# Kernel optimization log

Measured on AMD Instinct MI355X. Metric: run time of the kernel, lower is better.

Reference implementation:

```python
import jax, jax.numpy as jnp
import numpy as np

N, E, G = 20000, 160000, 32          # nodes, edges, graphs in batch
F_IN, H, P, C = 67, 2048, 1024, 18   # in_feat, hidden_feat, fc2 width, n_classifier
EPS = 1e-5
SLOPE = 0.01  # leaky_relu default negative slope


def setup_inputs() -> dict:
    key = jax.random.key(0)
    ks = jax.random.split(key, 24)
    w = lambda k, shape: (jax.random.normal(k, shape, jnp.float32) * 0.02)
    return {
        "h": jax.random.normal(ks[0], (N, F_IN), jnp.float32),
        "src": jax.random.randint(ks[1], (E,), 0, N),
        "dst": jax.random.randint(ks[2], (E,), 0, N),
        "gids": jnp.sort(jax.random.randint(ks[3], (N,), 0, G)),
        # SAGEConv layers: fc_self, fc_neigh (no per-fc bias), shared bias
        "ws1": w(ks[4], (F_IN, H)), "wn1": w(ks[5], (F_IN, H)), "b1": jnp.zeros((H,), jnp.float32),
        "ws2": w(ks[6], (H, H)),    "wn2": w(ks[7], (H, H)),    "b2": jnp.zeros((H,), jnp.float32),
        "ws3": w(ks[8], (H, H)),    "wn3": w(ks[9], (H, H)),    "b3": jnp.zeros((H,), jnp.float32),
        # batch norms (gamma, beta)
        "g1": jnp.ones((H,), jnp.float32), "be1": jnp.zeros((H,), jnp.float32),
        "g2": jnp.ones((H,), jnp.float32), "be2": jnp.zeros((H,), jnp.float32),
        "g3": jnp.ones((H,), jnp.float32), "be3": jnp.zeros((H,), jnp.float32),
        # MLP head
        "fw1": w(ks[10], (H, H)), "fb1": jnp.zeros((H,), jnp.float32),
        "fw2": w(ks[11], (H, P)), "fb2": jnp.zeros((P,), jnp.float32),
        "fw3": w(ks[12], (P, C)), "fb3": jnp.zeros((C,), jnp.float32),
    }


def _leaky(x):
    return jnp.where(x >= 0, x, SLOPE * x)


def _sage(x, src, dst, w_self, w_neigh, b):
    # DGL SAGEConv 'mean': mean of neighbor (src) features into dst, then linears.
    nsum = jax.ops.segment_sum(x[src], dst, num_segments=N)            # [N, F]
    deg = jax.ops.segment_sum(jnp.ones((E,), x.dtype), dst, num_segments=N)
    neigh = nsum / jnp.maximum(deg, 1.0)[:, None]                      # 0 for isolated
    return x @ w_self + neigh @ w_neigh + b


def _bn(x, gamma, beta):
    m = x.mean(0)
    v = x.var(0)
    return (x - m) * jax.lax.rsqrt(v + EPS) * gamma + beta


def reference(h, src, dst, gids,
              ws1, wn1, b1, g1, be1,
              ws2, wn2, b2, g2, be2,
              ws3, wn3, b3, g3, be3,
              fw1, fb1, fw2, fb2, fw3, fb3):
    x = _leaky(_bn(_sage(h, src, dst, ws1, wn1, b1), g1, be1))
    x = _leaky(_bn(_sage(x, src, dst, ws2, wn2, b2), g2, be2))
    x = _leaky(_bn(_sage(x, src, dst, ws3, wn3, b3), g3, be3))
    # mean pooling per graph
    gsum = jax.ops.segment_sum(x, gids, num_segments=G)                # [G, H]
    cnt = jax.ops.segment_sum(jnp.ones((N,), x.dtype), gids, num_segments=G)
    hg = gsum / jnp.maximum(cnt, 1.0)[:, None]
    # dropouts are identity in eval
    y = _leaky(hg @ fw1 + fb1)
    y = _leaky(y @ fw2 + fb2)
    return y @ fw3 + fb3
```

## Files before the change

### kernel.cpp

```cpp
#include <hip/hip_runtime.h>

typedef unsigned short u16;
typedef __attribute__((ext_vector_type(4))) float f32x4;
typedef __attribute__((ext_vector_type(8))) __bf16 bf16x8;
typedef __attribute__((ext_vector_type(8))) short s16x8;
typedef __attribute__((ext_vector_type(4))) u16 u16x4;

#define N_NODES 20000
#define N_EDGES 160000
#define N_GRAPH 32
#define F_IN 67
#define HID 2048
#define PW 1024
#define NCLS 18
#define MPAD 20096
#define MPAD2 20224
#define K1 192

__device__ __forceinline__ float bf2f(u16 u) {
    unsigned v = ((unsigned)u) << 16;
    float f; __builtin_memcpy(&f, &v, 4); return f;
}
__device__ __forceinline__ u16 f2bf(float f) {
    unsigned u; __builtin_memcpy(&u, &f, 4);
    u = (u + 0x7FFF + ((u >> 16) & 1)) >> 16;
    return (u16)u;
}
__device__ __forceinline__ int imax(int a, int b) { return a > b ? a : b; }

__device__ __forceinline__ void ld16(const u16* gptr, u16* lptr) {
    __builtin_amdgcn_global_load_lds(
        (const __attribute__((address_space(1))) unsigned int*)gptr,
        (__attribute__((address_space(3))) unsigned int*)lptr,
        16, 0, 0);
}

__global__ void k_hist(const int* __restrict__ dst, int* __restrict__ cnt) {
    int e = blockIdx.x * 256 + threadIdx.x;
    if (e < N_EDGES) atomicAdd(&cnt[dst[e]], 1);
}

__global__ void k_scan(const int* __restrict__ cnt, int* __restrict__ rowptr) {
    __shared__ int part[256];
    int t = threadIdx.x;
    const int per = (N_NODES + 255) / 256;
    int base = t * per;
    int s = 0;
    for (int i = 0; i < per; i++) { int idx = base + i; if (idx < N_NODES) s += cnt[idx]; }
    part[t] = s; __syncthreads();
    for (int off = 1; off < 256; off <<= 1) {
        int v = (t >= off) ? part[t - off] : 0;
        __syncthreads();
        part[t] += v;
        __syncthreads();
    }
    int running = (t == 0) ? 0 : part[t - 1];
    for (int i = 0; i < per; i++) {
        int idx = base + i;
        if (idx < N_NODES) { rowptr[idx] = running; running += cnt[idx]; }
    }
    if (t == 255) rowptr[N_NODES] = running;
}

__global__ void k_scatter(const int* __restrict__ src, const int* __restrict__ dst,
                          const int* __restrict__ rowptr, int* __restrict__ cursor,
                          int* __restrict__ csr) {
    int e = blockIdx.x * 256 + threadIdx.x;
    if (e < N_EDGES) {
        int d = dst[e];
        int p = atomicAdd(&cursor[d], 1);
        csr[rowptr[d] + p] = src[e];
    }
}

__global__ void k_w1t(const float* __restrict__ ws1, const float* __restrict__ wn1,
                      u16* __restrict__ w1t) {
    int n = blockIdx.x, t = threadIdx.x;
    float v = 0.f;
    if (t < F_IN) v = ws1[(size_t)t * HID + n];
    else if (t < 2 * F_IN) v = wn1[(size_t)(t - F_IN) * HID + n];
    w1t[(size_t)n * K1 + t] = f2bf(v);
}

__global__ void k_transpose2(const float* __restrict__ s0, const float* __restrict__ s1,
                             u16* __restrict__ dst) {
    __shared__ float tile[32][33];
    const float* src = blockIdx.z ? s1 : s0;
    int colofs = blockIdx.z ? HID : 0;
    int bx = blockIdx.x * 32, by = blockIdx.y * 32;
    int tx = threadIdx.x, ty = threadIdx.y;
#pragma unroll
    for (int i = 0; i < 32; i += 8)
        tile[ty + i][tx] = src[(size_t)(by + ty + i) * HID + bx + tx];
    __syncthreads();
#pragma unroll
    for (int i = 0; i < 32; i += 8)
        dst[(size_t)(bx + ty + i) * (2 * HID) + colofs + by + tx] = f2bf(tile[tx][ty + i]);
}

__global__ void k_agg1(const float* __restrict__ h, const int* __restrict__ rowptr,
                       const int* __restrict__ csr, u16* __restrict__ acat) {
    int n = blockIdx.x, t = threadIdx.x;
    if (t < F_IN) {
        acat[(size_t)n * K1 + t] = f2bf(h[(size_t)n * F_IN + t]);
    } else if (t < 2 * F_IN) {
        int c = t - F_IN;
        int e0 = rowptr[n], e1 = rowptr[n + 1];
        float a = 0.f;
        for (int e = e0; e < e1; e++) a += h[(size_t)csr[e] * F_IN + c];
        acat[(size_t)n * K1 + F_IN + c] = f2bf(a / (float)imax(e1 - e0, 1));
    }
}

__global__ __launch_bounds__(256)
void k_agg(const u16* __restrict__ x, const int* __restrict__ rowptr,
           const int* __restrict__ csr, u16* __restrict__ out) {
    int n = blockIdx.x, t = threadIdx.x;
    int e0 = rowptr[n], e1 = rowptr[n + 1];
    float acc[8] = {0, 0, 0, 0, 0, 0, 0, 0};
    for (int e = e0; e < e1; e++) {
        int s = csr[e];
        s16x8 v = *(const s16x8*)&x[(size_t)s * HID + t * 8];
#pragma unroll
        for (int j = 0; j < 8; j++) acc[j] += bf2f((u16)v[j]);
    }
    float inv = 1.0f / (float)imax(e1 - e0, 1);
    s16x8 o;
#pragma unroll
    for (int j = 0; j < 8; j++) o[j] = (short)f2bf(acc[j] * inv);
    *(s16x8*)&out[(size_t)n * HID + t * 8] = o;
}

__global__ __launch_bounds__(256)
void k_gemm(const u16* __restrict__ A0, const u16* __restrict__ A1, int ksplit,
            const u16* __restrict__ WT, u16* __restrict__ C,
            int ldA, int K, int ldC) {
    __shared__ u16 As[128 * 64];
    __shared__ u16 Bs[128 * 64];
    const int tid = threadIdx.x;
    const int lane = tid & 63;
    const int wave = tid >> 6;
    const int wr = (wave >> 1) * 64;
    const int wc = (wave & 1) * 64;
    const int lr = lane & 15;
    const int lk = (lane >> 4) * 8;
    const size_t row0 = (size_t)blockIdx.x * 128;
    const int col0 = blockIdx.y * 128;

    f32x4 acc[4][4];
#pragma unroll
    for (int i = 0; i < 4; i++)
#pragma unroll
        for (int j = 0; j < 4; j++) acc[i][j] = f32x4{0.f, 0.f, 0.f, 0.f};

    int rr[4], cc[4], lo[4];
#pragma unroll
    for (int i = 0; i < 4; i++) {
        int chunk = i * 256 + tid;
        rr[i] = chunk >> 3;
        cc[i] = (chunk & 7) * 8;
        lo[i] = (i * 256 + (wave << 6)) * 8;
    }
    size_t abase[4], bbase[4];
#pragma unroll
    for (int i = 0; i < 4; i++) {
        abase[i] = (row0 + rr[i]) * (size_t)ldA + cc[i];
        bbase[i] = ((size_t)col0 + rr[i]) * (size_t)K + cc[i];
    }

    for (int kt = 0; kt < K; kt += 64) {
        const u16* Asrc; int kc;
        if (kt < ksplit) { Asrc = A0; kc = kt; } else { Asrc = A1; kc = kt - ksplit; }
#pragma unroll
        for (int i = 0; i < 4; i++) {
            ld16(Asrc + abase[i] + kc, &As[lo[i]]);
            ld16(WT + bbase[i] + kt, &Bs[lo[i]]);
        }
        __syncthreads();
#pragma unroll
        for (int kk = 0; kk < 2; kk++) {
            bf16x8 af[4], bw[4];
#pragma unroll
            for (int i = 0; i < 4; i++)
                af[i] = *(const bf16x8*)&As[(wr + i * 16 + lr) * 64 + kk * 32 + lk];
#pragma unroll
            for (int j = 0; j < 4; j++)
                bw[j] = *(const bf16x8*)&Bs[(wc + j * 16 + lr) * 64 + kk * 32 + lk];
#pragma unroll
            for (int i = 0; i < 4; i++)
#pragma unroll
                for (int j = 0; j < 4; j++)
                    acc[i][j] = __builtin_amdgcn_mfma_f32_16x16x32_bf16(bw[j], af[i], acc[i][j], 0, 0, 0);
        }
        __syncthreads();
    }
#pragma unroll
    for (int i = 0; i < 4; i++) {
        size_t m = row0 + wr + i * 16 + lr;
#pragma unroll
        for (int j = 0; j < 4; j++) {
            int nb = col0 + wc + j * 16 + (lane >> 4) * 4;
            u16x4 o;
#pragma unroll
            for (int rg = 0; rg < 4; rg++) o[rg] = f2bf(acc[i][j][rg]);
            *(u16x4*)&C[m * (size_t)ldC + nb] = o;
        }
    }
}

#define VM4 asm volatile("s_waitcnt vmcnt(4)" ::: "memory")
#define VM2 asm volatile("s_waitcnt vmcnt(2)" ::: "memory")
#define VM0 asm volatile("s_waitcnt vmcnt(0)" ::: "memory")

#define STAGE_A(H) { const u16* as_ = (kt1 < 32 ? A0 : A1);                        \
    size_t ko_ = (size_t)(kt1 & 31) * 64 + swe;                                     \
    ld16(as_ + (row0 + 0 * 128 + (H) * 64 + r8) * 2048 + ko_,                       \
         LA + dbo + ((H) * 128 + 0 * 64 + r8) * 64 + ld8);                          \
    ld16(as_ + (row0 + 1 * 128 + (H) * 64 + r8) * 2048 + ko_,                       \
         LA + dbo + ((H) * 128 + 1 * 64 + r8) * 64 + ld8); }

#define STAGE_B(H) { size_t ko_ = (size_t)kt1 * 64 + swe;                           \
    ld16(WT + ((size_t)col0 + ((r8 >> 5)) * 64 + (H) * 32 + (r8 & 31)) * 4096 + ko_,\
         LB + dbo + ((H) * 128 + 0 * 64 + r8) * 64 + ld8);                          \
    ld16(WT + ((size_t)col0 + (2 + (r8 >> 5)) * 64 + (H) * 32 + (r8 & 31)) * 4096 + ko_,\
         LB + dbo + ((H) * 128 + 1 * 64 + r8) * 64 + ld8); }

#define RD_A(QM) {                                                                  \
    _Pragma("unroll") for (int f = 0; f < 4; ++f)                                   \
      _Pragma("unroll") for (int kk = 0; kk < 2; ++kk)                              \
        af[f][kk] = *(const bf16x8*)(bA + (QM) * 16384 + (wm * 64 + f * 16 + lr) * 128 \
                                     + ((kk * 64 + lg * 16) ^ rxor)); }

#define RD_B(DST, QN) {                                                             \
    _Pragma("unroll") for (int n = 0; n < 2; ++n)                                   \
      _Pragma("unroll") for (int kk = 0; kk < 2; ++kk)                              \
        DST[n][kk] = *(const bf16x8*)(bB + (QN) * 16384 + (wn * 32 + n * 16 + lr) * 128 \
                                     + ((kk * 64 + lg * 16) ^ rxor)); }

#define SYNC_MM(QM, QN, BW) {                                                       \
    __builtin_amdgcn_s_barrier();                                                   \
    __builtin_amdgcn_s_setprio(1);                                                  \
    _Pragma("unroll") for (int kk = 0; kk < 2; ++kk)                                \
      _Pragma("unroll") for (int f = 0; f < 4; ++f)                                 \
        _Pragma("unroll") for (int n = 0; n < 2; ++n)                               \
          acc[(QM) * 4 + f][(QN) * 2 + n] = __builtin_amdgcn_mfma_f32_16x16x32_bf16(\
              BW[n][kk], af[f][kk], acc[(QM) * 4 + f][(QN) * 2 + n], 0, 0, 0);      \
    __builtin_amdgcn_s_setprio(0); }

__global__ __launch_bounds__(512, 2)
void k_gemm256(const u16* __restrict__ A0, const u16* __restrict__ A1,
               const u16* __restrict__ WT, u16* __restrict__ C) {
    __shared__ u16 LA[2 * 256 * 64];
    __shared__ u16 LB[2 * 256 * 64];
    const int tid = threadIdx.x;
    const int lane = tid & 63;
    const int wave = tid >> 6;
    const int wm = wave >> 2, wn = wave & 3;
    const int lr = lane & 15, lg = lane >> 4;
    const int rxor = (lr & 7) << 4;

    const int g = (blockIdx.x & 7) * 79 + (blockIdx.x >> 3);
    const size_t row0 = (size_t)(g >> 3) * 256;
    const int col0 = (g & 7) * 256;

    const int r8 = tid >> 3;
    const int ld8 = (tid & 7) * 8;
    const int swe = ((ld8 * 2) ^ ((r8 & 7) << 4)) >> 1;

    f32x4 acc[8][4];
#pragma unroll
    for (int i = 0; i < 8; i++)
#pragma unroll
        for (int j = 0; j < 4; j++) acc[i][j] = f32x4{0.f, 0.f, 0.f, 0.f};

    {
        const int kt1 = 0; const int dbo = 0;
        STAGE_A(0) STAGE_B(0) STAGE_B(1) STAGE_A(1)
    }
    VM0;
    __builtin_amdgcn_s_barrier();

    bf16x8 af[4][2], bw[2][2], bw2[2][2];

    for (int t = 0; t < 63; ++t) {
        const char* bA = (const char*)LA + (t & 1) * 32768;
        const char* bB = (const char*)LB + (t & 1) * 32768;
        const int kt1 = t + 1;
        const int dbo = ((t + 1) & 1) * 16384;
        RD_A(0) RD_B(bw, 0) STAGE_A(0) VM4; SYNC_MM(0, 0, bw)
        RD_B(bw2, 1) STAGE_B(0) VM4; SYNC_MM(0, 1, bw2)
        RD_A(1) STAGE_B(1) SYNC_MM(1, 1, bw2)
        RD_B(bw, 0) STAGE_A(1) VM4; SYNC_MM(1, 0, bw)
    }
    {
        const char* bA = (const char*)LA + 32768;
        const char* bB = (const char*)LB + 32768;
        RD_A(0) RD_B(bw, 0) VM2; SYNC_MM(0, 0, bw)
        RD_B(bw2, 1) VM0; SYNC_MM(0, 1, bw2)
        RD_A(1) SYNC_MM(1, 1, bw2)
        RD_B(bw, 0) SYNC_MM(1, 0, bw)
    }

#pragma unroll
    for (int f = 0; f < 8; ++f) {
        size_t m = row0 + wm * 128 + f * 16 + lr;
#pragma unroll
        for (int n = 0; n < 4; ++n) {
            int cb = col0 + wn * 64 + n * 16 + lg * 4;
            u16x4 o;
#pragma unroll
            for (int rg = 0; rg < 4; ++rg) o[rg] = f2bf(acc[f][n][rg]);
            *(u16x4*)&C[m * HID + cb] = o;
        }
    }
}

__global__ __launch_bounds__(256)
void k_stats(const u16* __restrict__ x, float* __restrict__ ssum, float* __restrict__ ssq) {
    int t = threadIdx.x;
    int r0 = blockIdx.x * 100;
    float s[8] = {}, s2[8] = {};
    for (int i = 0; i < 100; ++i) {
        s16x8 v = *(const s16x8*)&x[(size_t)(r0 + i) * HID + t * 8];
#pragma unroll
        for (int j = 0; j < 8; ++j) { float f = bf2f((u16)v[j]); s[j] += f; s2[j] += f * f; }
    }
#pragma unroll
    for (int j = 0; j < 8; ++j) {
        atomicAdd(&ssum[t * 8 + j], s[j]);
        atomicAdd(&ssq[t * 8 + j], s2[j]);
    }
}

__global__ void k_bnleaky(const u16* __restrict__ xin,
                          const float* __restrict__ ssum, const float* __restrict__ ssq,
                          const float* __restrict__ gma, const float* __restrict__ bta,
                          u16* __restrict__ xout) {
    size_t eb = ((size_t)blockIdx.x * 256 + threadIdx.x) * 8;
    int col = (int)(eb & (HID - 1));
    s16x8 v = *(const s16x8*)&xin[eb];
    s16x8 o;
#pragma unroll
    for (int hq = 0; hq < 2; ++hq) {
        f32x4 su = *(const f32x4*)&ssum[col + hq * 4];
        f32x4 sq = *(const f32x4*)&ssq[col + hq * 4];
        f32x4 gm = *(const f32x4*)&gma[col + hq * 4];
        f32x4 bt = *(const f32x4*)&bta[col + hq * 4];
#pragma unroll
        for (int j = 0; j < 4; ++j) {
            float m = su[j] * (1.0f / N_NODES);
            float var = sq[j] * (1.0f / N_NODES) - m * m;
            float a = gm[j] * rsqrtf(var + 1e-5f);
            float d = bt[j] - m * a;
            float f = bf2f((u16)v[hq * 4 + j]) * a + d;
            f = f > 0.f ? f : 0.01f * f;
            o[hq * 4 + j] = (short)f2bf(f);
        }
    }
    *(s16x8*)&xout[eb] = o;
}

__global__ void k_bounds(const int* __restrict__ gids, int* __restrict__ gstart) {
    int t = threadIdx.x;
    if (t > N_GRAPH) return;
    int lo = 0, hi = N_NODES;
    while (lo < hi) { int mid = (lo + hi) >> 1; if (gids[mid] < t) lo = mid + 1; else hi = mid; }
    gstart[t] = lo;
}

__global__ void k_pool(const u16* __restrict__ x, const int* __restrict__ gstart,
                       float* __restrict__ hg) {
    int g = blockIdx.x;
    int col = blockIdx.y * 256 + threadIdx.x;
    int r0 = gstart[g], r1 = gstart[g + 1];
    float s = 0.f;
    for (int r = r0; r < r1; r++) s += bf2f(x[(size_t)r * HID + col]);
    hg[(size_t)g * HID + col] = s / (float)imax(r1 - r0, 1);
}

__global__ __launch_bounds__(256)
void k_mlp_part(const float* __restrict__ X, const float* __restrict__ W,
                float* __restrict__ Yp, int K, int Nc) {
    __shared__ float xs[32 * 256];
    int t = threadIdx.x;
    int kc = blockIdx.y;
    int n = blockIdx.x * 64 + (t & 63);
    int mg = t >> 6;
#pragma unroll
    for (int l = 0; l < 32; ++l) {
        int e = l * 256 + t;
        xs[e] = X[(size_t)(e >> 8) * K + kc * 256 + (e & 255)];
    }
    __syncthreads();
    float acc[8] = {};
    for (int k = 0; k < 256; ++k) {
        float wv = W[(size_t)(kc * 256 + k) * Nc + n];
#pragma unroll
        for (int i = 0; i < 8; ++i) acc[i] += xs[(mg * 8 + i) * 256 + k] * wv;
    }
#pragma unroll
    for (int i = 0; i < 8; ++i)
        Yp[(size_t)(kc * 32 + mg * 8 + i) * Nc + n] = acc[i];
}

__global__ void k_mlp_red(const float* __restrict__ Yp, const float* __restrict__ bias,
                          float* __restrict__ Y, int Nc, int leaky) {
    int idx = blockIdx.x * 256 + threadIdx.x;
    int n = idx % Nc;
    float s = 0.f;
#pragma unroll
    for (int kc = 0; kc < 8; ++kc) s += Yp[(size_t)kc * 32 * Nc + idx];
    float v = s + bias[n];
    if (leaky) v = v > 0.f ? v : 0.01f * v;
    Y[idx] = v;
}

__global__ void k_fc3(const float* __restrict__ y2, const float* __restrict__ fw3,
                      const float* __restrict__ fb3, float* __restrict__ out) {
    __shared__ float red[8][32];
    int m = blockIdx.x, t = threadIdx.x;
    int ch = t >> 5, c = t & 31;
    float s = 0.f;
    if (c < NCLS) {
        for (int j = 0; j < 128; ++j) {
            int k = ch * 128 + j;
            s += y2[(size_t)m * PW + k] * fw3[(size_t)k * NCLS + c];
        }
    }
    red[ch][c] = s;
    __syncthreads();
    if (t < NCLS) {
        float a = 0.f;
#pragma unroll
        for (int c2 = 0; c2 < 8; ++c2) a += red[c2][t];
        out[m * NCLS + t] = a + fb3[t];
    }
}

extern "C" void kernel_launch(void* const* d_in, const int* in_sizes, int n_in,
                              void* d_out, int out_size, void* d_ws, size_t ws_size,
                              hipStream_t stream) {
    const float* h   = (const float*)d_in[0];
    const int* src   = (const int*)d_in[1];
    const int* dst   = (const int*)d_in[2];
    const int* gids  = (const int*)d_in[3];
    const float* ws1 = (const float*)d_in[4];
    const float* wn1 = (const float*)d_in[5];
    const float* ws2 = (const float*)d_in[7];
    const float* wn2 = (const float*)d_in[8];
    const float* ws3 = (const float*)d_in[10];
    const float* wn3 = (const float*)d_in[11];
    const float* g1  = (const float*)d_in[13];
    const float* be1 = (const float*)d_in[14];
    const float* g2  = (const float*)d_in[15];
    const float* be2 = (const float*)d_in[16];
    const float* g3  = (const float*)d_in[17];
    const float* be3 = (const float*)d_in[18];
    const float* fw1 = (const float*)d_in[19];
    const float* fb1 = (const float*)d_in[20];
    const float* fw2 = (const float*)d_in[21];
    const float* fb2 = (const float*)d_in[22];
    const float* fw3 = (const float*)d_in[23];
    const float* fb3 = (const float*)d_in[24];
    float* out = (float*)d_out;
    (void)in_sizes; (void)n_in; (void)out_size;

    char* base = (char*)d_ws;
    size_t off = 0;
    auto alloc = [&](size_t b) -> char* {
        char* p = base + off;
        off += (b + 255) & ~(size_t)255;
        return p;
    };
    u16* BUF0 = (u16*)alloc((size_t)MPAD2 * HID * 2);
    u16* BUF1 = (u16*)alloc((size_t)MPAD2 * HID * 2);
    u16* BUF2 = (u16*)alloc((size_t)MPAD2 * HID * 2);
    u16* WT   = (u16*)alloc((size_t)HID * 2 * HID * 2);
    int* cnt    = (int*)alloc(N_NODES * 4);
    int* rowptr = (int*)alloc((N_NODES + 1) * 4);
    int* cursor = (int*)alloc(N_NODES * 4);
    int* csr    = (int*)alloc(N_EDGES * 4);
    float* ssum = (float*)alloc(HID * 4);
    float* ssq  = (float*)alloc(HID * 4);
    int* gstart = (int*)alloc(64 * 4);
    float* hg = (float*)alloc((size_t)N_GRAPH * HID * 4);
    float* y1 = (float*)alloc((size_t)N_GRAPH * HID * 4);
    float* y2 = (float*)alloc((size_t)N_GRAPH * PW * 4);
    u16* ACAT = (u16*)((char*)BUF2);
    u16* W1T  = (u16*)((char*)BUF2 + (size_t)MPAD * K1 * 2);
    float* Yp = (float*)((char*)BUF2);

    if (off > ws_size) return;

    hipMemsetAsync(cnt, 0, N_NODES * 4, stream);
    hipMemsetAsync(cursor, 0, N_NODES * 4, stream);
    hipMemsetAsync(ACAT, 0, (size_t)MPAD * K1 * 2, stream);

    k_hist<<<(N_EDGES + 255) / 256, 256, 0, stream>>>(dst, cnt);
    k_scan<<<1, 256, 0, stream>>>(cnt, rowptr);
    k_scatter<<<(N_EDGES + 255) / 256, 256, 0, stream>>>(src, dst, rowptr, cursor, csr);

    k_w1t<<<HID, K1, 0, stream>>>(ws1, wn1, W1T);
    k_agg1<<<N_NODES, 192, 0, stream>>>(h, rowptr, csr, ACAT);

    dim3 gg(MPAD / 128, HID / 128);
    dim3 tb(32, 8);
    k_gemm<<<gg, 256, 0, stream>>>(ACAT, ACAT, K1, W1T, BUF0, K1, K1, HID);
    hipMemsetAsync(ssum, 0, 2 * HID * 4, stream);
    k_stats<<<200, 256, 0, stream>>>(BUF0, ssum, ssq);
    k_bnleaky<<<20000, 256, 0, stream>>>(BUF0, ssum, ssq, g1, be1, BUF1);
    k_transpose2<<<dim3(64, 64, 2), tb, 0, stream>>>(ws2, wn2, WT);
    k_agg<<<N_NODES, 256, 0, stream>>>(BUF1, rowptr, csr, BUF2);
    k_gemm256<<<632, 512, 0, stream>>>(BUF1, BUF2, WT, BUF0);
    hipMemsetAsync(ssum, 0, 2 * HID * 4, stream);
    k_stats<<<200, 256, 0, stream>>>(BUF0, ssum, ssq);
    k_bnleaky<<<20000, 256, 0, stream>>>(BUF0, ssum, ssq, g2, be2, BUF1);
    k_transpose2<<<dim3(64, 64, 2), tb, 0, stream>>>(ws3, wn3, WT);
    k_agg<<<N_NODES, 256, 0, stream>>>(BUF1, rowptr, csr, BUF2);
    k_gemm256<<<632, 512, 0, stream>>>(BUF1, BUF2, WT, BUF0);
    hipMemsetAsync(ssum, 0, 2 * HID * 4, stream);
    k_stats<<<200, 256, 0, stream>>>(BUF0, ssum, ssq);
    k_bnleaky<<<20000, 256, 0, stream>>>(BUF0, ssum, ssq, g3, be3, BUF1);
    k_bounds<<<1, 64, 0, stream>>>(gids, gstart);
    k_pool<<<dim3(N_GRAPH, HID / 256), 256, 0, stream>>>(BUF1, gstart, hg);
    k_mlp_part<<<dim3(HID / 64, 8), 256, 0, stream>>>(hg, fw1, Yp, HID, HID);
    k_mlp_red<<<(N_GRAPH * HID) / 256, 256, 0, stream>>>(Yp, fb1, y1, HID, 1);
    k_mlp_part<<<dim3(PW / 64, 8), 256, 0, stream>>>(y1, fw2, Yp, HID, PW);
    k_mlp_red<<<(N_GRAPH * PW) / 256, 256, 0, stream>>>(Yp, fb2, y2, PW, 1);
    k_fc3<<<N_GRAPH, 256, 0, stream>>>(y2, fw3, fb3, out);
}
```

Measured before the change: 1.553 ms.

## Fuse batch-norm statistics into GEMM epilogue and reuse 256-tile GEMM for layer one

New measurement: 1.408 ms. 1.1x faster.

```diff
diff --git a/kernel.cpp b/kernel.cpp
--- a/kernel.cpp
+++ b/kernel.cpp
@@ -13,7 +13,6 @@
 #define HID 2048
 #define PW 1024
 #define NCLS 18
-#define MPAD 20096
 #define MPAD2 20224
 #define K1 192
 
@@ -131,98 +130,22 @@
     *(s16x8*)&out[(size_t)n * HID + t * 8] = o;
 }
 
-__global__ __launch_bounds__(256)
-void k_gemm(const u16* __restrict__ A0, const u16* __restrict__ A1, int ksplit,
-            const u16* __restrict__ WT, u16* __restrict__ C,
-            int ldA, int K, int ldC) {
-    __shared__ u16 As[128 * 64];
-    __shared__ u16 Bs[128 * 64];
-    const int tid = threadIdx.x;
-    const int lane = tid & 63;
-    const int wave = tid >> 6;
-    const int wr = (wave >> 1) * 64;
-    const int wc = (wave & 1) * 64;
-    const int lr = lane & 15;
-    const int lk = (lane >> 4) * 8;
-    const size_t row0 = (size_t)blockIdx.x * 128;
-    const int col0 = blockIdx.y * 128;
-
-    f32x4 acc[4][4];
-#pragma unroll
-    for (int i = 0; i < 4; i++)
-#pragma unroll
-        for (int j = 0; j < 4; j++) acc[i][j] = f32x4{0.f, 0.f, 0.f, 0.f};
-
-    int rr[4], cc[4], lo[4];
-#pragma unroll
-    for (int i = 0; i < 4; i++) {
-        int chunk = i * 256 + tid;
-        rr[i] = chunk >> 3;
-        cc[i] = (chunk & 7) * 8;
-        lo[i] = (i * 256 + (wave << 6)) * 8;
-    }
-    size_t abase[4], bbase[4];
-#pragma unroll
-    for (int i = 0; i < 4; i++) {
-        abase[i] = (row0 + rr[i]) * (size_t)ldA + cc[i];
-        bbase[i] = ((size_t)col0 + rr[i]) * (size_t)K + cc[i];
-    }
-
-    for (int kt = 0; kt < K; kt += 64) {
-        const u16* Asrc; int kc;
-        if (kt < ksplit) { Asrc = A0; kc = kt; } else { Asrc = A1; kc = kt - ksplit; }
-#pragma unroll
-        for (int i = 0; i < 4; i++) {
-            ld16(Asrc + abase[i] + kc, &As[lo[i]]);
-            ld16(WT + bbase[i] + kt, &Bs[lo[i]]);
-        }
-        __syncthreads();
-#pragma unroll
-        for (int kk = 0; kk < 2; kk++) {
-            bf16x8 af[4], bw[4];
-#pragma unroll
-            for (int i = 0; i < 4; i++)
-                af[i] = *(const bf16x8*)&As[(wr + i * 16 + lr) * 64 + kk * 32 + lk];
-#pragma unroll
-            for (int j = 0; j < 4; j++)
-                bw[j] = *(const bf16x8*)&Bs[(wc + j * 16 + lr) * 64 + kk * 32 + lk];
-#pragma unroll
-            for (int i = 0; i < 4; i++)
-#pragma unroll
-                for (int j = 0; j < 4; j++)
-                    acc[i][j] = __builtin_amdgcn_mfma_f32_16x16x32_bf16(bw[j], af[i], acc[i][j], 0, 0, 0);
-        }
-        __syncthreads();
-    }
-#pragma unroll
-    for (int i = 0; i < 4; i++) {
-        size_t m = row0 + wr + i * 16 + lr;
-#pragma unroll
-        for (int j = 0; j < 4; j++) {
-            int nb = col0 + wc + j * 16 + (lane >> 4) * 4;
-            u16x4 o;
-#pragma unroll
-            for (int rg = 0; rg < 4; rg++) o[rg] = f2bf(acc[i][j][rg]);
-            *(u16x4*)&C[m * (size_t)ldC + nb] = o;
-        }
-    }
-}
-
 #define VM4 asm volatile("s_waitcnt vmcnt(4)" ::: "memory")
 #define VM2 asm volatile("s_waitcnt vmcnt(2)" ::: "memory")
 #define VM0 asm volatile("s_waitcnt vmcnt(0)" ::: "memory")
 
-#define STAGE_A(H) { const u16* as_ = (kt1 < 32 ? A0 : A1);                        \
-    size_t ko_ = (size_t)(kt1 & 31) * 64 + swe;                                     \
-    ld16(as_ + (row0 + 0 * 128 + (H) * 64 + r8) * 2048 + ko_,                       \
+#define STAGE_A(H) { const u16* as_; int ktl_;                                      \
+    if (kt1 < kskt) { as_ = A0; ktl_ = kt1; } else { as_ = A1; ktl_ = kt1 - kskt; } \
+    size_t ko_ = (size_t)ktl_ * 64 + swe;                                           \
+    ld16(as_ + (row0 + 0 * 128 + (H) * 64 + r8) * (size_t)lda + ko_,                \
          LA + dbo + ((H) * 128 + 0 * 64 + r8) * 64 + ld8);                          \
-    ld16(as_ + (row0 + 1 * 128 + (H) * 64 + r8) * 2048 + ko_,                       \
+    ld16(as_ + (row0 + 1 * 128 + (H) * 64 + r8) * (size_t)lda + ko_,                \
          LA + dbo + ((H) * 128 + 1 * 64 + r8) * 64 + ld8); }
 
 #define STAGE_B(H) { size_t ko_ = (size_t)kt1 * 64 + swe;                           \
-    ld16(WT + ((size_t)col0 + ((r8 >> 5)) * 64 + (H) * 32 + (r8 & 31)) * 4096 + ko_,\
+    ld16(WT + ((size_t)col0 + ((r8 >> 5)) * 64 + (H) * 32 + (r8 & 31)) * (size_t)ldb + ko_,\
          LB + dbo + ((H) * 128 + 0 * 64 + r8) * 64 + ld8);                          \
-    ld16(WT + ((size_t)col0 + (2 + (r8 >> 5)) * 64 + (H) * 32 + (r8 & 31)) * 4096 + ko_,\
+    ld16(WT + ((size_t)col0 + (2 + (r8 >> 5)) * 64 + (H) * 32 + (r8 & 31)) * (size_t)ldb + ko_,\
          LB + dbo + ((H) * 128 + 1 * 64 + r8) * 64 + ld8); }
 
 #define RD_A(QM) {                                                                  \
@@ -249,7 +172,9 @@
 
 __global__ __launch_bounds__(512, 2)
 void k_gemm256(const u16* __restrict__ A0, const u16* __restrict__ A1,
-               const u16* __restrict__ WT, u16* __restrict__ C) {
+               const u16* __restrict__ WT, u16* __restrict__ C,
+               float* __restrict__ ssum, float* __restrict__ ssq,
+               int nkt, int kskt, int lda, int ldb) {
     __shared__ u16 LA[2 * 256 * 64];
     __shared__ u16 LB[2 * 256 * 64];
     const int tid = threadIdx.x;
@@ -282,7 +207,7 @@
 
     bf16x8 af[4][2], bw[2][2], bw2[2][2];
 
-    for (int t = 0; t < 63; ++t) {
+    for (int t = 0; t < nkt - 1; ++t) {
         const char* bA = (const char*)LA + (t & 1) * 32768;
         const char* bB = (const char*)LB + (t & 1) * 32768;
         const int kt1 = t + 1;
@@ -293,8 +218,8 @@
         RD_B(bw, 0) STAGE_A(1) VM4; SYNC_MM(1, 0, bw)
     }
     {
-        const char* bA = (const char*)LA + 32768;
-        const char* bB = (const char*)LB + 32768;
+        const char* bA = (const char*)LA + ((nkt - 1) & 1) * 32768;
+        const char* bB = (const char*)LB + ((nkt - 1) & 1) * 32768;
         RD_A(0) RD_B(bw, 0) VM2; SYNC_MM(0, 0, bw)
         RD_B(bw2, 1) VM0; SYNC_MM(0, 1, bw2)
         RD_A(1) SYNC_MM(1, 1, bw2)
@@ -313,22 +238,24 @@
             *(u16x4*)&C[m * HID + cb] = o;
         }
     }
-}
-
-__global__ __launch_bounds__(256)
-void k_stats(const u16* __restrict__ x, float* __restrict__ ssum, float* __restrict__ ssq) {
-    int t = threadIdx.x;
-    int r0 = blockIdx.x * 100;
-    float s[8] = {}, s2[8] = {};
-    for (int i = 0; i < 100; ++i) {
-        s16x8 v = *(const s16x8*)&x[(size_t)(r0 + i) * HID + t * 8];
-#pragma unroll
-        for (int j = 0; j < 8; ++j) { float f = bf2f((u16)v[j]); s[j] += f; s2[j] += f * f; }
-    }
-#pragma unroll
-    for (int j = 0; j < 8; ++j) {
-        atomicAdd(&ssum[t * 8 + j], s[j]);
-        atomicAdd(&ssq[t * 8 + j], s2[j]);
+#pragma unroll
+    for (int n = 0; n < 4; ++n) {
+#pragma unroll
+        for (int rg = 0; rg < 4; ++rg) {
+            float s = 0.f, s2 = 0.f;
+#pragma unroll
+            for (int f = 0; f < 8; ++f) { float v = acc[f][n][rg]; s += v; s2 += v * v; }
+#pragma unroll
+            for (int mk = 1; mk < 16; mk <<= 1) {
+                s += __shfl_xor(s, mk, 64);
+                s2 += __shfl_xor(s2, mk, 64);
+            }
+            if (lr == 0) {
+                int cb = col0 + wn * 64 + n * 16 + lg * 4 + rg;
+                atomicAdd(&ssum[cb], s);
+                atomicAdd(&ssq[cb], s2);
+            }
+        }
     }
 }
 
@@ -487,14 +414,16 @@
     float* y1 = (float*)alloc((size_t)N_GRAPH * HID * 4);
     float* y2 = (float*)alloc((size_t)N_GRAPH * PW * 4);
     u16* ACAT = (u16*)((char*)BUF2);
-    u16* W1T  = (u16*)((char*)BUF2 + (size_t)MPAD * K1 * 2);
+    u16* W1T  = (u16*)((char*)BUF2 + (size_t)MPAD2 * K1 * 2);
     float* Yp = (float*)((char*)BUF2);
 
     if (off > ws_size) return;
 
     hipMemsetAsync(cnt, 0, N_NODES * 4, stream);
     hipMemsetAsync(cursor, 0, N_NODES * 4, stream);
-    hipMemsetAsync(ACAT, 0, (size_t)MPAD * K1 * 2, stream);
+    hipMemsetAsync(ACAT, 0, (size_t)MPAD2 * K1 * 2, stream);
+    hipMemsetAsync(BUF1 + (size_t)N_NODES * HID, 0, (size_t)(MPAD2 - N_NODES) * HID * 2, stream);
+    hipMemsetAsync(BUF2 + (size_t)N_NODES * HID, 0, (size_t)(MPAD2 - N_NODES) * HID * 2, stream);
 
     k_hist<<<(N_EDGES + 255) / 256, 256, 0, stream>>>(dst, cnt);
     k_scan<<<1, 256, 0, stream>>>(cnt, rowptr);
@@ -503,23 +432,19 @@
     k_w1t<<<HID, K1, 0, stream>>>(ws1, wn1, W1T);
     k_agg1<<<N_NODES, 192, 0, stream>>>(h, rowptr, csr, ACAT);
 
-    dim3 gg(MPAD / 128, HID / 128);
     dim3 tb(32, 8);
-    k_gemm<<<gg, 256, 0, stream>>>(ACAT, ACAT, K1, W1T, BUF0, K1, K1, HID);
     hipMemsetAsync(ssum, 0, 2 * HID * 4, stream);
-    k_stats<<<200, 256, 0, stream>>>(BUF0, ssum, ssq);
+    k_gemm256<<<632, 512, 0, stream>>>(ACAT, ACAT, W1T, BUF0, ssum, ssq, 3, 3, K1, K1);
     k_bnleaky<<<20000, 256, 0, stream>>>(BUF0, ssum, ssq, g1, be1, BUF1);
     k_transpose2<<<dim3(64, 64, 2), tb, 0, stream>>>(ws2, wn2, WT);
     k_agg<<<N_NODES, 256, 0, stream>>>(BUF1, rowptr, csr, BUF2);
-    k_gemm256<<<632, 512, 0, stream>>>(BUF1, BUF2, WT, BUF0);
     hipMemsetAsync(ssum, 0, 2 * HID * 4, stream);
-    k_stats<<<200, 256, 0, stream>>>(BUF0, ssum, ssq);
+    k_gemm256<<<632, 512, 0, stream>>>(BUF1, BUF2, WT, BUF0, ssum, ssq, 64, 32, HID, 2 * HID);
     k_bnleaky<<<20000, 256, 0, stream>>>(BUF0, ssum, ssq, g2, be2, BUF1);
     k_transpose2<<<dim3(64, 64, 2), tb, 0, stream>>>(ws3, wn3, WT);
     k_agg<<<N_NODES, 256, 0, stream>>>(BUF1, rowptr, csr, BUF2);
-    k_gemm256<<<632, 512, 0, stream>>>(BUF1, BUF2, WT, BUF0);
     hipMemsetAsync(ssum, 0, 2 * HID * 4, stream);
-    k_stats<<<200, 256, 0, stream>>>(BUF0, ssum, ssq);
+    k_gemm256<<<632, 512, 0, stream>>>(BUF1, BUF2, WT, BUF0, ssum, ssq, 64, 32, HID, 2 * HID);
     k_bnleaky<<<20000, 256, 0, stream>>>(BUF0, ssum, ssq, g3, be3, BUF1);
     k_bounds<<<1, 64, 0, stream>>>(gids, gstart);
     k_pool<<<dim3(N_GRAPH, HID / 256), 256, 0, stream>>>(BUF1, gstart, hg);
```
